# Kernel optimization log

Measured on AMD Instinct MI355X. Metric: run time of the kernel, lower is better.

The kernel has to match this reference:

```python
import jax, jax.numpy as jnp
import numpy as np

ALPHA = 0.7            # _cfg.alpha  (abnormal-growth threshold ratio)
SIGMA = 0.1            # _cfg.sigma  (gaussian splatting bandwidth)
MIN_MINING_STEP = 50   # _cfg.min_mining_step
NCROPS = 2             # pfu crop count (uncrop = mean over crops)


def setup_inputs() -> dict:
    key = jax.random.key(0)
    k1, k2 = jax.random.split(key)
    B, T, C = 64, 2048, NCROPS
    scores = jax.random.normal(k1, (B * C, T), dtype=jnp.float32)
    # balanced bag: first half abnormal (labels==1), matching bat_div == bs//2
    labels = jnp.concatenate([jnp.ones(B // 2, jnp.int32), jnp.zeros(B // 2, jnp.int32)])
    point_label = (jax.random.uniform(k2, (B, T)) < 0.004).astype(jnp.int32)
    seqlen = jnp.full((B,), T, dtype=jnp.int32)  # full length -> no padding path
    return {"scores": scores, "labels": labels, "point_label": point_label,
            "seqlen": seqlen, "step": 100}


def _mine_one(score, plabel, valid_len):
    """gaussian_kernel_mining for one video. score/plabel: [T].
    Grows labels outward from each anchor while score >= ALPHA*score[anchor],
    stopping at the first failure (segmented cumulative-AND, resetting at anchors)."""
    T = score.shape[0]
    is_anchor = plabel > 0

    def scan_dir(s, a):
        def step(carry, xs):
            ok, anch, has = carry          # chain-unbroken flag, last anchor score, anchor seen
            sj, aj = xs
            cond = sj >= ALPHA * anch
            grown = ok & cond & has        # position mined by growth in this direction
            ok2 = jnp.where(aj, True, grown)
            anch2 = jnp.where(aj, sj, anch)
            return (ok2, anch2, has | aj), grown
        init = (jnp.asarray(True), jnp.float32(0.0), jnp.asarray(False))
        _, g = jax.lax.scan(step, init, (s, a))
        return g

    g_fwd = scan_dir(score, is_anchor) & (jnp.arange(T) < valid_len)  # rightward growth
    g_bwd = scan_dir(score[::-1], is_anchor[::-1])[::-1]              # leftward growth
    return (is_anchor | g_fwd | g_bwd).astype(jnp.float32)


def _splat_table(T):
    """[p, i] normalized gaussian weights; identical for every video since N==T."""
    i = jnp.arange(T, dtype=jnp.float32)
    h = 2.0 * (i - 1.0) / (T - 1.0) - 1.0
    d = h[None, :] - h[:, None]
    W = jnp.exp(-d * d / (2.0 * SIGMA * SIGMA)) / (SIGMA * jnp.sqrt(2.0 * jnp.pi))
    wmin = W.min(axis=1, keepdims=True)
    wmax = W.max(axis=1, keepdims=True)
    return jnp.where(wmax > wmin, (W - wmin) / (wmax - wmin), jnp.ones_like(W))


def _splat_one(mask, Wn):
    """temporal_gaussian_splatting for one video: max over anchor rows, then min-max."""
    any_a = mask.any()
    temp = jnp.max(jnp.where(mask[:, None], Wn, -jnp.inf), axis=0)
    tmin, tmax = temp.min(), temp.max()
    temp_n = jnp.where(tmax > tmin, (temp - tmin) / (tmax - tmin), temp)
    return jnp.where(any_a, temp_n, jnp.zeros_like(temp))


def reference(scores, labels, point_label, seqlen, step):
    BC, T = scores.shape
    B = BC // NCROPS
    nb = B // 2  # bat_div == bs//2: first half abnormal
    # sigmoid then uncrop (mean over crops)
    probs = jax.nn.sigmoid(scores).reshape(B, NCROPS, T).mean(axis=1)
    abn_scores = probs[:nb]                      # unbag abnormal half
    abn_pl = point_label[:nb]
    # mining runs on detached scores -> pseudo labels carry no gradient
    s_det = jax.lax.stop_gradient(abn_scores)
    abn_kernel = jax.vmap(_mine_one)(s_det, abn_pl, seqlen[:nb])
    base = abn_pl.astype(jnp.float32) if step < MIN_MINING_STEP else abn_kernel
    Wn = _splat_table(T)
    rendered = jax.vmap(lambda m: _splat_one(m > 0, Wn))(base)
    # BCELoss(reduction='none').mean() with rendered as target
    per_elem = -(rendered * jnp.log(abn_scores) + (1.0 - rendered) * jnp.log1p(-abn_scores))
    return jnp.mean(per_elem)
```

## Files before the change

### kernel.cpp

```cpp
#include <hip/hip_runtime.h>
#include <cstdint>
#include <climits>
#include <cmath>

#define ALPHA 0.7f
#define SIGMA 0.1f
#define MIN_MINING_STEP 50

constexpr int TT    = 2048;
constexpr int NTH   = 512;
constexpr int EPT   = TT / NTH;
constexpr int NWAVE = NTH / 64;

__device__ __forceinline__ void dual_maxscan(int (&v)[EPT], int (&w)[EPT],
                                             int& exV, int& exW, int* sW) {
    const int tid = threadIdx.x, lane = tid & 63, wid = tid >> 6;
#pragma unroll
    for (int k = 1; k < EPT; ++k) {
        v[k] = max(v[k], v[k - 1]);
        w[k] = max(w[k], w[k - 1]);
    }
    int tv = v[EPT - 1], tw = w[EPT - 1];
#pragma unroll
    for (int off = 1; off < 64; off <<= 1) {
        int nv = __shfl_up(tv, off), nw = __shfl_up(tw, off);
        if (lane >= off) { tv = max(tv, nv); tw = max(tw, nw); }
    }
    if (lane == 63) { sW[wid] = tv; sW[NWAVE + wid] = tw; }
    __syncthreads();
    int ev = INT_MIN, ew = INT_MIN;
    for (int q = 0; q < wid; ++q) {
        ev = max(ev, sW[q]);
        ew = max(ew, sW[NWAVE + q]);
    }
    int uv = __shfl_up(tv, 1), uw = __shfl_up(tw, 1);
    if (lane > 0) { ev = max(ev, uv); ew = max(ew, uw); }
    exV = ev; exW = ew;
#pragma unroll
    for (int k = 0; k < EPT; ++k) {
        v[k] = max(v[k], ev);
        w[k] = max(w[k], ew);
    }
}

__device__ __forceinline__ float waveRedMin(float v) {
#pragma unroll
    for (int off = 32; off > 0; off >>= 1) v = fminf(v, __shfl_xor(v, off));
    return v;
}
__device__ __forceinline__ float waveRedSum(float v) {
#pragma unroll
    for (int off = 32; off > 0; off >>= 1) v += __shfl_xor(v, off);
    return v;
}

__global__ __launch_bounds__(NTH) void glance_fused(
    const float* __restrict__ scores,
    const int*   __restrict__ point_label,
    const int*   __restrict__ seqlen,
    const int*   __restrict__ step_p,
    float*       __restrict__ partial,
    int C)
{
    __shared__ float sS[TT];
    __shared__ int   sM[TT];
    __shared__ int   sW[6 * NWAVE];
    __shared__ float sRmin[NWAVE];
    __shared__ float sRsum[NWAVE];

    const int b = blockIdx.x, tid = threadIdx.x, lane = tid & 63, wid = tid >> 6;

    const float invC = 1.0f / (float)C;
    for (int q4 = tid; q4 < TT / 4; q4 += NTH) {
        float4 acc = make_float4(0.f, 0.f, 0.f, 0.f);
        for (int c = 0; c < C; ++c) {
            const float4 x = ((const float4*)(scores + ((size_t)(b * C + c)) * TT))[q4];
            acc.x += 1.0f / (1.0f + __expf(-x.x));
            acc.y += 1.0f / (1.0f + __expf(-x.y));
            acc.z += 1.0f / (1.0f + __expf(-x.z));
            acc.w += 1.0f / (1.0f + __expf(-x.w));
        }
        const int4 p = ((const int4*)(point_label + (size_t)b * TT))[q4];
        const int t = q4 * 4;
        sS[t + 0] = acc.x * invC;  sM[t + 0] = (p.x > 0) ? 1 : 0;
        sS[t + 1] = acc.y * invC;  sM[t + 1] = (p.y > 0) ? 1 : 0;
        sS[t + 2] = acc.z * invC;  sM[t + 2] = (p.z > 0) ? 1 : 0;
        sS[t + 3] = acc.w * invC;  sM[t + 3] = (p.w > 0) ? 1 : 0;
    }
    const int stepv = step_p[0];
    const int vlen  = seqlen[b];
    __syncthreads();

    const int j0 = tid * EPT;

    if (stepv >= MIN_MINING_STEP) {
        int va[EPT], wa[EPT]; int exA, exB;
#pragma unroll
        for (int k = 0; k < EPT; ++k) {
            const int j = j0 + k;
            va[k] = sM[j] ? j : -1;
            wa[k] = sM[TT - 1 - j] ? j : -1;
        }
        dual_maxscan(va, wa, exA, exB, sW);

        int vf[EPT], wf[EPT]; int exF, exG;
        int qf[EPT], qb[EPT];
#pragma unroll
        for (int k = 0; k < EPT; ++k) {
            const int j  = j0 + k;
            const int qF = (k == 0) ? exA : va[k - 1];
            const int qB = (k == 0) ? exB : wa[k - 1];
            qf[k] = qF; qb[k] = qB;
            bool cF = false, cB = false;
            if (qF >= 0) cF = sS[j]          >= ALPHA * sS[qF];
            if (qB >= 0) cB = sS[TT - 1 - j] >= ALPHA * sS[TT - 1 - qB];
            vf[k] = cF ? -1 : j;
            wf[k] = cB ? -1 : j;
        }
        dual_maxscan(vf, wf, exF, exG, sW + 2 * NWAVE);

#pragma unroll
        for (int k = 0; k < EPT; ++k) {
            const int j = j0 + k;
            const bool gF = (qf[k] >= 0) && (vf[k] <= qf[k]) && (j < vlen);
            const bool gB = (qb[k] >= 0) && (wf[k] <= qb[k]);
            if (gF) sM[j] = 1;
            if (gB) sM[TT - 1 - j] = 1;
        }
        __syncthreads();
    }

    int vn[EPT], wn[EPT]; int exN, exO;
#pragma unroll
    for (int k = 0; k < EPT; ++k) {
        const int j = j0 + k;
        vn[k] = sM[j] ? j : -1;
        wn[k] = sM[TT - 1 - j] ? j : -1;
    }
    dual_maxscan(vn, wn, exN, exO, sW + 4 * NWAVE);

#pragma unroll
    for (int k = 0; k < EPT; ++k) {
        const int j  = j0 + k;
        const int dB = (wn[k] >= 0) ? min(j - wn[k], 4096) : 4096;
        sM[TT - 1 - j] = dB;
    }
    if (tid == NTH - 1) sW[0] = (vn[EPT - 1] >= 0) ? 1 : 0;
    __syncthreads();
    const bool any = (sW[0] != 0);

    const float KK = 2.0f / ((float)(TT - 1) * (float)(TT - 1) * SIGMA * SIGMA);
    float tempv[EPT];
    float tmn = INFINITY;
#pragma unroll
    for (int k = 0; k < EPT; ++k) {
        const int j  = j0 + k;
        const int dF = (vn[k] >= 0) ? min(j - vn[k], 4096) : 4096;
        const int d  = min(dF, sM[j]);
        const float tv = __expf(-KK * (float)(d * d));
        tempv[k] = tv;
        tmn = fminf(tmn, tv);
    }
    tmn = waveRedMin(tmn);
    if (lane == 0) sRmin[wid] = tmn;
    __syncthreads();
    tmn = sRmin[0];
    for (int w = 1; w < NWAVE; ++w) tmn = fminf(tmn, sRmin[w]);

    const bool norm = any && (tmn < 1.0f);
    const float inv = norm ? 1.0f / (1.0f - tmn) : 0.0f;
    float lsum = 0.0f;
#pragma unroll
    for (int k = 0; k < EPT; ++k) {
        float r = 0.0f;
        if (any) r = norm ? (tempv[k] - tmn) * inv : tempv[k];
        const float s = sS[j0 + k];
        lsum += -(r * __logf(s) + (1.0f - r) * __logf(1.0f - s));
    }
    lsum = waveRedSum(lsum);
    if (lane == 0) sRsum[wid] = lsum;
    __syncthreads();
    if (tid == 0) {
        float tot = 0.0f;
        for (int w = 0; w < NWAVE; ++w) tot += sRsum[w];
        partial[b] = tot;
    }
}

__global__ __launch_bounds__(64) void glance_reduce(
    const float* __restrict__ partial, float* __restrict__ out, int nb, float invN)
{
    float v = ((int)threadIdx.x < nb) ? partial[threadIdx.x] : 0.0f;
#pragma unroll
    for (int off = 32; off > 0; off >>= 1) v += __shfl_down(v, off);
    if (threadIdx.x == 0) out[0] = v * invN;
}

extern "C" void kernel_launch(void* const* d_in, const int* in_sizes, int n_in,
                              void* d_out, int out_size, void* d_ws, size_t ws_size,
                              hipStream_t stream) {
    (void)n_in; (void)out_size; (void)ws_size;
    const float* scores      = (const float*)d_in[0];
    const int*   point_label = (const int*)d_in[2];
    const int*   seqlen      = (const int*)d_in[3];
    const int*   step_p      = (const int*)d_in[4];

    const int B  = in_sizes[1];
    const int T  = in_sizes[2] / B;
    const int C  = in_sizes[0] / (B * T);
    const int nb = B / 2;

    float* partial = (float*)d_ws;

    glance_fused<<<nb, NTH, 0, stream>>>(scores, point_label, seqlen, step_p,
                                         partial, C);
    glance_reduce<<<1, 64, 0, stream>>>(partial, (float*)d_out, nb,
                                        1.0f / (float)(nb * T));
}
```

Baseline: 67.82 us.

## Fold normalization algebraically into single reduction pass and atomic-accumulate loss

```diff
diff --git a/kernel.cpp b/kernel.cpp
--- a/kernel.cpp
+++ b/kernel.cpp
@@ -43,15 +43,8 @@
     }
 }
 
-__device__ __forceinline__ float waveRedMin(float v) {
-#pragma unroll
-    for (int off = 32; off > 0; off >>= 1) v = fminf(v, __shfl_xor(v, off));
-    return v;
-}
-__device__ __forceinline__ float waveRedSum(float v) {
-#pragma unroll
-    for (int off = 32; off > 0; off >>= 1) v += __shfl_xor(v, off);
-    return v;
+__global__ __launch_bounds__(64) void zero_out(float* __restrict__ out) {
+    if (threadIdx.x == 0) out[0] = 0.0f;
 }
 
 __global__ __launch_bounds__(NTH) void glance_fused(
@@ -59,16 +52,18 @@
     const int*   __restrict__ point_label,
     const int*   __restrict__ seqlen,
     const int*   __restrict__ step_p,
-    float*       __restrict__ partial,
-    int C)
+    float*       out,
+    int C, float invN)
 {
     __shared__ float sS[TT];
     __shared__ int   sM[TT];
     __shared__ int   sW[6 * NWAVE];
-    __shared__ float sRmin[NWAVE];
-    __shared__ float sRsum[NWAVE];
+    __shared__ float sR[4 * NWAVE];
 
     const int b = blockIdx.x, tid = threadIdx.x, lane = tid & 63, wid = tid >> 6;
+
+    const int stepv = step_p[0];
+    const int vlen  = seqlen[b];
 
     const float invC = 1.0f / (float)C;
     for (int q4 = tid; q4 < TT / 4; q4 += NTH) {
@@ -87,8 +82,6 @@
         sS[t + 2] = acc.z * invC;  sM[t + 2] = (p.z > 0) ? 1 : 0;
         sS[t + 3] = acc.w * invC;  sM[t + 3] = (p.w > 0) ? 1 : 0;
     }
-    const int stepv = step_p[0];
-    const int vlen  = seqlen[b];
     __syncthreads();
 
     const int j0 = tid * EPT;
@@ -142,64 +135,67 @@
 #pragma unroll
     for (int k = 0; k < EPT; ++k) {
         const int j  = j0 + k;
-        const int dB = (wn[k] >= 0) ? min(j - wn[k], 4096) : 4096;
+        const int dB = (wn[k] >= 0) ? (j - wn[k]) : 4096;
         sM[TT - 1 - j] = dB;
     }
-    if (tid == NTH - 1) sW[0] = (vn[EPT - 1] >= 0) ? 1 : 0;
-    __syncthreads();
-    const bool any = (sW[0] != 0);
+    __syncthreads();
+
+    const bool any = (vn[0] >= 0) || (sM[j0] < 4096);
 
     const float KK = 2.0f / ((float)(TT - 1) * (float)(TT - 1) * SIGMA * SIGMA);
-    float tempv[EPT];
-    float tmn = INFINITY;
+    float tmn = INFINITY, L0 = 0.0f, Su = 0.0f, Stu = 0.0f;
 #pragma unroll
     for (int k = 0; k < EPT; ++k) {
         const int j  = j0 + k;
-        const int dF = (vn[k] >= 0) ? min(j - vn[k], 4096) : 4096;
+        const int dF = (vn[k] >= 0) ? (j - vn[k]) : 4096;
         const int d  = min(dF, sM[j]);
-        const float tv = __expf(-KK * (float)(d * d));
-        tempv[k] = tv;
+        const float tv  = __expf(-KK * (float)(d * d));
+        const float s   = sS[j];
+        const float ls  = __logf(s);
+        const float l1s = __logf(1.0f - s);
+        const float u   = ls - l1s;
         tmn = fminf(tmn, tv);
-    }
-    tmn = waveRedMin(tmn);
-    if (lane == 0) sRmin[wid] = tmn;
-    __syncthreads();
-    tmn = sRmin[0];
-    for (int w = 1; w < NWAVE; ++w) tmn = fminf(tmn, sRmin[w]);
-
-    const bool norm = any && (tmn < 1.0f);
-    const float inv = norm ? 1.0f / (1.0f - tmn) : 0.0f;
-    float lsum = 0.0f;
-#pragma unroll
-    for (int k = 0; k < EPT; ++k) {
-        float r = 0.0f;
-        if (any) r = norm ? (tempv[k] - tmn) * inv : tempv[k];
-        const float s = sS[j0 + k];
-        lsum += -(r * __logf(s) + (1.0f - r) * __logf(1.0f - s));
-    }
-    lsum = waveRedSum(lsum);
-    if (lane == 0) sRsum[wid] = lsum;
+        L0 += l1s;
+        Su += u;
+        Stu += tv * u;
+    }
+#pragma unroll
+    for (int off = 32; off > 0; off >>= 1) {
+        tmn = fminf(tmn, __shfl_xor(tmn, off));
+        L0  += __shfl_xor(L0,  off);
+        Su  += __shfl_xor(Su,  off);
+        Stu += __shfl_xor(Stu, off);
+    }
+    if (lane == 0) {
+        sR[wid * 4 + 0] = tmn;
+        sR[wid * 4 + 1] = L0;
+        sR[wid * 4 + 2] = Su;
+        sR[wid * 4 + 3] = Stu;
+    }
     __syncthreads();
     if (tid == 0) {
-        float tot = 0.0f;
-        for (int w = 0; w < NWAVE; ++w) tot += sRsum[w];
-        partial[b] = tot;
-    }
-}
-
-__global__ __launch_bounds__(64) void glance_reduce(
-    const float* __restrict__ partial, float* __restrict__ out, int nb, float invN)
-{
-    float v = ((int)threadIdx.x < nb) ? partial[threadIdx.x] : 0.0f;
-#pragma unroll
-    for (int off = 32; off > 0; off >>= 1) v += __shfl_down(v, off);
-    if (threadIdx.x == 0) out[0] = v * invN;
+        float m = sR[0], a = sR[1], su = sR[2], st = sR[3];
+        for (int w = 1; w < NWAVE; ++w) {
+            m = fminf(m, sR[w * 4 + 0]);
+            a  += sR[w * 4 + 1];
+            su += sR[w * 4 + 2];
+            st += sR[w * 4 + 3];
+        }
+        float loss;
+        if (!any)             loss = -a;
+        else if (m >= 1.0f)   loss = -(su + a);
+        else {
+            const float inv = 1.0f / (1.0f - m);
+            loss = -a - inv * (st - m * su);
+        }
+        atomicAdd(out, loss * invN);
+    }
 }
 
 extern "C" void kernel_launch(void* const* d_in, const int* in_sizes, int n_in,
                               void* d_out, int out_size, void* d_ws, size_t ws_size,
                               hipStream_t stream) {
-    (void)n_in; (void)out_size; (void)ws_size;
+    (void)n_in; (void)out_size; (void)d_ws; (void)ws_size;
     const float* scores      = (const float*)d_in[0];
     const int*   point_label = (const int*)d_in[2];
     const int*   seqlen      = (const int*)d_in[3];
@@ -210,10 +206,8 @@
     const int C  = in_sizes[0] / (B * T);
     const int nb = B / 2;
 
-    float* partial = (float*)d_ws;
-
+    zero_out<<<1, 64, 0, stream>>>((float*)d_out);
     glance_fused<<<nb, NTH, 0, stream>>>(scores, point_label, seqlen, step_p,
-                                         partial, C);
-    glance_reduce<<<1, 64, 0, stream>>>(partial, (float*)d_out, nb,
-                                        1.0f / (float)(nb * T));
-}
+                                         (float*)d_out, C,
+                                         1.0f / (float)(nb * T));
+}
```

Measured after the change: 68.61 us. About the same (+1.2%).
